# Kernel tuning notes

Hardware: AMD Instinct MI355X
Metric: run time of the kernel (lower is better)

Reference implementation:

```python
import jax, jax.numpy as jnp
import numpy as np

B, S, D = 4, 2048, 1024
H = 16
DK = D // H  # 64, dim_k == dim_v
FF = 4096
EPS = 1e-5


def layer_norm(x, g, b):
    mu = jnp.mean(x, axis=-1, keepdims=True)
    var = jnp.mean(jnp.square(x - mu), axis=-1, keepdims=True)
    return (x - mu) * jax.lax.rsqrt(var + EPS) * g + b


def setup_inputs() -> dict:
    key = jax.random.key(0)
    ks = jax.random.split(key, 16)
    s = 0.02
    return {
        "src": jax.random.normal(ks[0], (B, S, D), jnp.float32),
        # per-head Q/K/V projections (stacked over heads)
        "wq": jax.random.normal(ks[1], (H, D, DK), jnp.float32) * s,
        "bq": jnp.zeros((H, DK), jnp.float32),
        "wk": jax.random.normal(ks[2], (H, D, DK), jnp.float32) * s,
        "bk": jnp.zeros((H, DK), jnp.float32),
        "wv": jax.random.normal(ks[3], (H, D, DK), jnp.float32) * s,
        "bv": jnp.zeros((H, DK), jnp.float32),
        # output projection: concat(H*DK) -> D
        "wo": jax.random.normal(ks[4], (H * DK, D), jnp.float32) * s,
        "bo": jnp.zeros((D,), jnp.float32),
        "ln1_g": jnp.ones((D,), jnp.float32),
        "ln1_b": jnp.zeros((D,), jnp.float32),
        # FFN
        "w1": jax.random.normal(ks[5], (D, FF), jnp.float32) * s,
        "b1": jnp.zeros((FF,), jnp.float32),
        "w2": jax.random.normal(ks[6], (FF, D), jnp.float32) * s,
        "b2": jnp.zeros((D,), jnp.float32),
        "ln2_g": jnp.ones((D,), jnp.float32),
        "ln2_b": jnp.zeros((D,), jnp.float32),
    }


def reference(src, wq, bq, wk, bk, wv, bv, wo, bo, ln1_g, ln1_b,
              w1, b1, w2, b2, ln2_g, ln2_b):
    # per-head projections: [B,S,D] x [H,D,K] -> [B,H,S,K]
    q = jnp.einsum('bsd,hdk->bhsk', src, wq) + bq[None, :, None, :]
    k = jnp.einsum('bsd,hdk->bhsk', src, wk) + bk[None, :, None, :]
    v = jnp.einsum('bsd,hdk->bhsk', src, wv) + bv[None, :, None, :]
    scale = 1.0 / jnp.sqrt(jnp.float32(DK))
    scores = jnp.einsum('bhsk,bhtk->bhst', q, k) * scale  # [B,H,S,S]
    attn = jax.nn.softmax(scores, axis=-1)
    o = jnp.einsum('bhst,bhtv->bhsv', attn, v)            # [B,H,S,DK]
    o = o.transpose(0, 2, 1, 3).reshape(B, S, H * DK)      # concat heads
    attn_out = o @ wo + bo
    x = layer_norm(src + attn_out, ln1_g, ln1_b)
    ff = jax.nn.relu(x @ w1 + b1) @ w2 + b2
    return layer_norm(x + ff, ln2_g, ln2_b)
```

## Files before the change

kernel.cpp:

```cpp
#include <hip/hip_runtime.h>

typedef __bf16 bf16;
typedef __bf16 bf16x8 __attribute__((ext_vector_type(8)));
typedef __bf16 bf16x4 __attribute__((ext_vector_type(4)));
typedef float  f32x4  __attribute__((ext_vector_type(4)));
typedef float  f32x16 __attribute__((ext_vector_type(16)));
typedef unsigned int u32;
typedef int i32x2 __attribute__((ext_vector_type(2)));

#define NB 4
#define NS 2048
#define ND 1024
#define NH 16
#define NDK 64
#define NFF 4096
#define NM (NB*NS)

__device__ __forceinline__ void load_lds16(const void* g, void* l) {
  __builtin_amdgcn_global_load_lds(
      (const __attribute__((address_space(1))) void*)g,
      (__attribute__((address_space(3))) void*)l, 16, 0, 0);
}

__device__ __forceinline__ u32 pack2(float a, float b) {
  union { bf16 h[2]; u32 u; } z;
  z.h[0] = (bf16)a; z.h[1] = (bf16)b;
  return z.u;
}

__device__ __forceinline__ i32x2 pswap(u32 a, u32 b) {
#if __has_builtin(__builtin_amdgcn_permlane32_swap)
  return __builtin_amdgcn_permlane32_swap((int)a, (int)b, false, false);
#else
  u32 x = a, y = b;
  asm volatile("v_permlane32_swap_b32 %0, %1" : "+v"(x), "+v"(y));
  i32x2 r; r[0] = (int)x; r[1] = (int)y; return r;
#endif
}

__global__ __launch_bounds__(256)
void cvt_f32_bf16(const float* __restrict__ in, bf16* __restrict__ out, int n) {
  int i = (blockIdx.x * 256 + threadIdx.x) * 4;
  if (i < n) {
    float4 v = *(const float4*)&in[i];
    bf16x4 o;
    o[0] = (bf16)v.x; o[1] = (bf16)v.y; o[2] = (bf16)v.z; o[3] = (bf16)v.w;
    *(bf16x4*)&out[i] = o;
  }
}

__global__ __launch_bounds__(256)
void transpose_cvt(const float* __restrict__ in, bf16* __restrict__ out,
                   int R, int C, size_t in_bs, size_t out_bs) {
  __shared__ float t[32][33];
  int bx = blockIdx.x, by = blockIdx.y, bz = blockIdx.z;
  const float* ip = in + (size_t)bz * in_bs + (size_t)(bx * 32) * C + by * 32;
  bf16* op = out + (size_t)bz * out_bs + (size_t)(by * 32) * R + bx * 32;
  int x = threadIdx.x & 31, y = threadIdx.x >> 5;
#pragma unroll
  for (int yy = 0; yy < 32; yy += 8)
    t[y + yy][x] = ip[(size_t)(y + yy) * C + x];
  __syncthreads();
#pragma unroll
  for (int yy = 0; yy < 32; yy += 8)
    op[(size_t)(y + yy) * R + x] = (bf16)t[x][y + yy];
}

__global__ __launch_bounds__(256)
void transpose_v(const bf16* __restrict__ v, bf16* __restrict__ vT) {
  __shared__ bf16 t[64][72];
  int st = blockIdx.x;
  int bh = blockIdx.y;
  const bf16* ip = v + ((size_t)bh * NS + st * 64) * NDK;
  bf16* op = vT + (size_t)bh * NDK * NS + st * 64;
  int tid = threadIdx.x;
#pragma unroll
  for (int c = tid; c < 512; c += 256) {
    int r = c >> 3, q = c & 7;
    bf16x8 d = *(const bf16x8*)&ip[(size_t)r * NDK + q * 8];
#pragma unroll
    for (int j = 0; j < 8; j++) t[r][q * 8 + j] = d[j];
  }
  __syncthreads();
#pragma unroll
  for (int c = tid; c < 512; c += 256) {
    int dv = c >> 3, sq = c & 7;
    bf16x8 d;
#pragma unroll
    for (int j = 0; j < 8; j++) d[j] = t[sq * 8 + j][dv];
    *(bf16x8*)&op[(size_t)dv * NS + sq * 8] = d;
  }
}

template<int EPI>
__global__ __launch_bounds__(256)
void gemm_bt(const bf16* __restrict__ A, const bf16* __restrict__ Bt,
             const float* __restrict__ bias0, const float* __restrict__ bias1,
             const float* __restrict__ bias2, void* __restrict__ out0,
             int M, int N, int K) {
  __shared__ __align__(16) bf16 lA[128 * 32];
  __shared__ __align__(16) bf16 lB[128 * 32];
  const int tid = threadIdx.x;
  const int lane = tid & 63;
  const int w = tid >> 6;
  const int wr = w >> 1, wc = w & 1;
  const int blane = lane & 15, glane = lane >> 4;
  const int bm = blockIdx.x * 128;
  const int bn = blockIdx.y * 128;

  f32x4 acc[4][4] = {};
  const bf16* aBase = A + (size_t)bm * K;
  const bf16* bBase = Bt + (size_t)bn * K;
  const int c0 = tid, c1 = tid + 256;

  for (int kt = 0; kt < K; kt += 32) {
    const bf16* ag = aBase + kt;
    const bf16* bg = bBase + kt;
    load_lds16(ag + (size_t)(c0 >> 2) * K + (c0 & 3) * 8, &lA[c0 * 8]);
    load_lds16(ag + (size_t)(c1 >> 2) * K + (c1 & 3) * 8, &lA[c1 * 8]);
    load_lds16(bg + (size_t)(c0 >> 2) * K + (c0 & 3) * 8, &lB[c0 * 8]);
    load_lds16(bg + (size_t)(c1 >> 2) * K + (c1 & 3) * 8, &lB[c1 * 8]);
    __syncthreads();
    bf16x8 af[4], bfr[4];
#pragma unroll
    for (int m = 0; m < 4; m++) {
      int row = wr * 64 + m * 16 + blane;
      af[m] = *(const bf16x8*)&lA[row * 32 + glane * 8];
    }
#pragma unroll
    for (int n = 0; n < 4; n++) {
      int row = wc * 64 + n * 16 + blane;
      bfr[n] = *(const bf16x8*)&lB[row * 32 + glane * 8];
    }
#pragma unroll
    for (int m = 0; m < 4; m++)
#pragma unroll
      for (int n = 0; n < 4; n++)
        acc[m][n] = __builtin_amdgcn_mfma_f32_16x16x32_bf16(af[m], bfr[n], acc[m][n], 0, 0, 0);
    __syncthreads();
  }

#pragma unroll
  for (int m = 0; m < 4; m++) {
#pragma unroll
    for (int n = 0; n < 4; n++) {
      int col = bn + wc * 64 + n * 16 + blane;
      if (EPI == 0) {
        int sel = col >> 10;
        int hh = (col & 1023) >> 6;
        int dv = col & 63;
        const float* bp = (sel == 0) ? bias0 : (sel == 1) ? bias1 : bias2;
        float bias = bp[col & 1023];
        bf16* outb = (bf16*)out0 + (size_t)sel * NB * NH * NS * NDK;
#pragma unroll
        for (int i = 0; i < 4; i++) {
          int row = bm + wr * 64 + m * 16 + glane * 4 + i;
          int b_ = row >> 11, s_ = row & 2047;
          outb[(((size_t)(b_ * NH + hh) * NS + s_) * NDK) + dv] = (bf16)(acc[m][n][i] + bias);
        }
      } else if (EPI == 1) {
        float bias = bias0[col];
#pragma unroll
        for (int i = 0; i < 4; i++) {
          int row = bm + wr * 64 + m * 16 + glane * 4 + i;
          float v = acc[m][n][i] + bias;
          v = v > 0.f ? v : 0.f;
          ((bf16*)out0)[(size_t)row * N + col] = (bf16)v;
        }
      } else {
        float bias = bias0[col];
#pragma unroll
        for (int i = 0; i < 4; i++) {
          int row = bm + wr * 64 + m * 16 + glane * 4 + i;
          ((float*)out0)[(size_t)row * N + col] = acc[m][n][i] + bias;
        }
      }
    }
  }
}

__global__ __launch_bounds__(256)
void flash_attn3(const bf16* __restrict__ q, const bf16* __restrict__ k,
                 const bf16* __restrict__ vT, bf16* __restrict__ o) {
  __shared__ __align__(16) bf16 lK[2][64 * 64];
  __shared__ __align__(16) bf16 lV[2][64 * 64];
  const int tid = threadIdx.x, lane = tid & 63, w = tid >> 6;
  const int ql = lane & 31, hi = lane >> 5;
  const int bh = blockIdx.y, qt = blockIdx.x;
  const size_t hb = (size_t)bh * NS * NDK;
  const int qrow = qt * 128 + w * 32 + ql;

  bf16x8 qf[4];
#pragma unroll
  for (int ks = 0; ks < 4; ks++)
    qf[ks] = *(const bf16x8*)&q[hb + (size_t)qrow * NDK + ks * 16 + hi * 8];

  const int r0 = tid >> 3, s0 = ((tid & 7) ^ (r0 & 7)) * 8;
  const int r1 = r0 + 32, s1 = ((tid & 7) ^ (r1 & 7)) * 8;
  const bf16* k0 = k + hb + (size_t)r0 * NDK + s0;
  const bf16* k1 = k + hb + (size_t)r1 * NDK + s1;
  const bf16* v0 = vT + hb + (size_t)r0 * NS + s0;
  const bf16* v1 = vT + hb + (size_t)r1 * NS + s1;

  f32x16 o0 = {}, o1 = {};
  float mR = -3e38f, lR = 0.f;
  const float cl2 = 0.18033688f;

  load_lds16(k0, &lK[0][tid * 8]);
  load_lds16(k1, &lK[0][(tid + 256) * 8]);
  load_lds16(v0, &lV[0][tid * 8]);
  load_lds16(v1, &lV[0][(tid + 256) * 8]);
  __syncthreads();

  const char* lKc = (const char*)&lK[0][0];
  const char* lVc = (const char*)&lV[0][0];
  const int swz = (ql & 7) << 4;

  for (int t = 0; t < NS / 64; t++) {
    const int cur = t & 1;
    if (t < NS / 64 - 1) {
      const size_t ko = (size_t)(t + 1) * 64 * NDK;
      const int vo = (t + 1) * 64;
      load_lds16(k0 + ko, &lK[cur ^ 1][tid * 8]);
      load_lds16(k1 + ko, &lK[cur ^ 1][(tid + 256) * 8]);
      load_lds16(v0 + vo, &lV[cur ^ 1][tid * 8]);
      load_lds16(v1 + vo, &lV[cur ^ 1][(tid + 256) * 8]);
    }
    const char* Kb = lKc + cur * 8192;
    const char* Vb = lVc + cur * 8192;

    f32x16 st0 = {}, st1 = {};
    __builtin_amdgcn_s_setprio(1);
#pragma unroll
    for (int ks = 0; ks < 4; ks++) {
      int byt = (32 * ks + 16 * hi) ^ swz;
      bf16x8 kf0 = *(const bf16x8*)(Kb + ql * 128 + byt);
      bf16x8 kf1 = *(const bf16x8*)(Kb + (32 + ql) * 128 + byt);
      st0 = __builtin_amdgcn_mfma_f32_32x32x16_bf16(kf0, qf[ks], st0, 0, 0, 0);
      st1 = __builtin_amdgcn_mfma_f32_32x32x16_bf16(kf1, qf[ks], st1, 0, 0, 0);
    }
    __builtin_amdgcn_s_setprio(0);

    float mx = st0[0];
#pragma unroll
    for (int r = 1; r < 16; r++) mx = fmaxf(mx, st0[r]);
#pragma unroll
    for (int r = 0; r < 16; r++) mx = fmaxf(mx, st1[r]);
    {
      i32x2 xr = pswap((u32)__float_as_int(mx), (u32)__float_as_int(mx));
      float prt = __int_as_float(hi ? xr[0] : xr[1]);
      mx = fmaxf(mx, prt);
    }

    if (!__all((mx - mR) * cl2 <= 8.0f)) {
      float mn = fmaxf(mR, mx);
      float al = exp2f((mR - mn) * cl2);
      lR *= al;
#pragma unroll
      for (int r = 0; r < 16; r++) { o0[r] *= al; o1[r] *= al; }
      mR = mn;
    }
    float cmn = mR * cl2;
    float ls = 0.f;
#pragma unroll
    for (int r = 0; r < 16; r++) { float p = exp2f(fmaf(st0[r], cl2, -cmn)); st0[r] = p; ls += p; }
#pragma unroll
    for (int r = 0; r < 16; r++) { float p = exp2f(fmaf(st1[r], cl2, -cmn)); st1[r] = p; ls += p; }
    {
      i32x2 sr = pswap((u32)__float_as_int(ls), (u32)__float_as_int(ls));
      float lsp = __int_as_float(hi ? sr[0] : sr[1]);
      float lo_ = hi ? lsp : ls, hi_ = hi ? ls : lsp;
      lR += lo_ + hi_;
    }

#pragma unroll
    for (int tt = 0; tt < 2; tt++) {
      f32x16 stv = (tt == 0) ? st0 : st1;
      u32 wv[8];
#pragma unroll
      for (int i = 0; i < 8; i++) wv[i] = pack2(stv[2 * i], stv[2 * i + 1]);
#pragma unroll
      for (int kk = 0; kk < 2; kk++) {
        const int base = 4 * kk;
        i32x2 e0 = pswap(wv[base + 0], wv[base + 2]);
        i32x2 e1 = pswap(wv[base + 1], wv[base + 3]);
        union { u32 u[4]; bf16x8 v; } pf;
        pf.u[0] = (u32)e0[0];
        pf.u[1] = (u32)e1[0];
        pf.u[2] = (u32)e0[1];
        pf.u[3] = (u32)e1[1];
        const int ks = 2 * tt + kk;
        int vbyt = (32 * ks + 16 * hi) ^ swz;
        bf16x8 vf0 = *(const bf16x8*)(Vb + ql * 128 + vbyt);
        bf16x8 vf1 = *(const bf16x8*)(Vb + (32 + ql) * 128 + vbyt);
        __builtin_amdgcn_s_setprio(1);
        o0 = __builtin_amdgcn_mfma_f32_32x32x16_bf16(vf0, pf.v, o0, 0, 0, 0);
        o1 = __builtin_amdgcn_mfma_f32_32x32x16_bf16(vf1, pf.v, o1, 0, 0, 0);
        __builtin_amdgcn_s_setprio(0);
      }
    }
    __syncthreads();
  }

  float invl = 1.0f / lR;
  int b_ = bh >> 4, h_ = bh & 15;
  bf16* ob = o + ((size_t)(b_ * NS + qrow) * (NH * NDK)) + h_ * NDK;
#pragma unroll
  for (int rp = 0; rp < 8; rp++) {
    int dv = 8 * (rp >> 1) + 2 * (rp & 1) + 4 * hi;
    *(u32*)&ob[dv]      = pack2(o0[2 * rp] * invl, o0[2 * rp + 1] * invl);
    *(u32*)&ob[dv + 32] = pack2(o1[2 * rp] * invl, o1[2 * rp + 1] * invl);
  }
}

template<int WB>
__global__ __launch_bounds__(256)
void ln_res(const float* __restrict__ a, const float* __restrict__ b,
            const float* __restrict__ g, const float* __restrict__ be,
            float* __restrict__ y, bf16* __restrict__ yb) {
  int row = blockIdx.x;
  int tid = threadIdx.x;
  const float4* a4 = (const float4*)(a + (size_t)row * ND);
  const float4* b4 = (const float4*)(b + (size_t)row * ND);
  float4 av = a4[tid], bv = b4[tid];
  float x0 = av.x + bv.x, x1 = av.y + bv.y, x2 = av.z + bv.z, x3 = av.w + bv.w;
  float s = x0 + x1 + x2 + x3;
  float qq_ = x0 * x0 + x1 * x1 + x2 * x2 + x3 * x3;
#pragma unroll
  for (int d = 1; d < 64; d <<= 1) { s += __shfl_xor(s, d); qq_ += __shfl_xor(qq_, d); }
  __shared__ float ss[4], sq[4];
  int w = tid >> 6, lane = tid & 63;
  if (lane == 0) { ss[w] = s; sq[w] = qq_; }
  __syncthreads();
  s = ss[0] + ss[1] + ss[2] + ss[3];
  qq_ = sq[0] + sq[1] + sq[2] + sq[3];
  float mu = s * (1.0f / ND);
  float var = qq_ * (1.0f / ND) - mu * mu;
  float rs = 1.0f / sqrtf(var + 1e-5f);
  const float4* g4 = (const float4*)g;
  const float4* e4 = (const float4*)be;
  float4 gv = g4[tid], ev = e4[tid];
  float o0 = (x0 - mu) * rs * gv.x + ev.x;
  float o1 = (x1 - mu) * rs * gv.y + ev.y;
  float o2 = (x2 - mu) * rs * gv.z + ev.z;
  float o3 = (x3 - mu) * rs * gv.w + ev.w;
  float4 ov = {o0, o1, o2, o3};
  *(float4*)(y + (size_t)row * ND + tid * 4) = ov;
  if (WB) {
    bf16x4 wv;
    wv[0] = (bf16)o0; wv[1] = (bf16)o1; wv[2] = (bf16)o2; wv[3] = (bf16)o3;
    *(bf16x4*)&yb[(size_t)row * ND + tid * 4] = wv;
  }
}

extern "C" void kernel_launch(void* const* d_in, const int* in_sizes, int n_in,
                              void* d_out, int out_size, void* d_ws, size_t ws_size,
                              hipStream_t stream) {
  const float* src = (const float*)d_in[0];
  const float* wq  = (const float*)d_in[1];
  const float* bq  = (const float*)d_in[2];
  const float* wk  = (const float*)d_in[3];
  const float* bk  = (const float*)d_in[4];
  const float* wv  = (const float*)d_in[5];
  const float* bv  = (const float*)d_in[6];
  const float* wo  = (const float*)d_in[7];
  const float* bo  = (const float*)d_in[8];
  const float* g1  = (const float*)d_in[9];
  const float* be1 = (const float*)d_in[10];
  const float* w1  = (const float*)d_in[11];
  const float* b1  = (const float*)d_in[12];
  const float* w2  = (const float*)d_in[13];
  const float* b2  = (const float*)d_in[14];
  const float* g2  = (const float*)d_in[15];
  const float* be2 = (const float*)d_in[16];

  char* ws = (char*)d_ws;
  bf16*  srcb  = (bf16*)(ws + 0);
  bf16*  wqkvT = (bf16*)(ws + 16777216);
  bf16*  woT   = (bf16*)(ws + 23068672);
  bf16*  w1T   = (bf16*)(ws + 25165824);
  bf16*  w2T   = (bf16*)(ws + 33554432);
  bf16*  qkv   = (bf16*)(ws + 41943040);
  bf16*  vT    = (bf16*)(ws + 92274688);
  bf16*  attno = (bf16*)(ws + 109051904);
  float* tmpf  = (float*)(ws + 125829120);
  float* x     = (float*)(ws + 159383552);
  bf16*  xb    = (bf16*)(ws + 192937984);
  bf16*  hbuf  = qkv;

  const size_t QKVSZ = (size_t)NB * NH * NS * NDK;

  cvt_f32_bf16<<<8192, 256, 0, stream>>>(src, srcb, NM * ND);
  transpose_cvt<<<dim3(32, 2, 16), 256, 0, stream>>>(wq, wqkvT,               1024, 64, 65536, 65536);
  transpose_cvt<<<dim3(32, 2, 16), 256, 0, stream>>>(wk, wqkvT + 1024 * 1024, 1024, 64, 65536, 65536);
  transpose_cvt<<<dim3(32, 2, 16), 256, 0, stream>>>(wv, wqkvT + 2048 * 1024, 1024, 64, 65536, 65536);
  transpose_cvt<<<dim3(32, 32, 1), 256, 0, stream>>>(wo, woT, 1024, 1024, 0, 0);
  transpose_cvt<<<dim3(32, 128, 1), 256, 0, stream>>>(w1, w1T, 1024, 4096, 0, 0);
  transpose_cvt<<<dim3(128, 32, 1), 256, 0, stream>>>(w2, w2T, 4096, 1024, 0, 0);

  gemm_bt<0><<<dim3(64, 24), 256, 0, stream>>>(srcb, wqkvT, bq, bk, bv, qkv, NM, 3072, 1024);
  transpose_v<<<dim3(32, 64), 256, 0, stream>>>(qkv + 2 * QKVSZ, vT);
  flash_attn3<<<dim3(16, 64), 256, 0, stream>>>(qkv, qkv + QKVSZ, vT, attno);
  gemm_bt<2><<<dim3(64, 8), 256, 0, stream>>>(attno, woT, bo, nullptr, nullptr, tmpf, NM, 1024, 1024);
  ln_res<1><<<8192, 256, 0, stream>>>(src, tmpf, g1, be1, x, xb);
  gemm_bt<1><<<dim3(64, 32), 256, 0, stream>>>(xb, w1T, b1, nullptr, nullptr, hbuf, NM, 4096, 1024);
  gemm_bt<2><<<dim3(64, 8), 256, 0, stream>>>(hbuf, w2T, b2, nullptr, nullptr, tmpf, NM, 1024, 4096);
  ln_res<0><<<8192, 256, 0, stream>>>(x, tmpf, g2, be2, (float*)d_out, nullptr);
}
```

Measured before the change: 523.5 us.

## Replace GEMM kernel with 256-row tiled, double-buffered, 8-wave pipelined MFMA GEMM

Replaces the simple 128x128 single-buffered GEMM with a 512-thread kernel using 256xBN tiles, K=64 steps, double-buffered LDS with XOR swizzling, and an interleaved schedule of LDS loads, global-to-LDS prefetch and MFMA quarters separated by barriers and setprio hints. It also remaps blocks in an XCD-aware order to improve L2 locality. This targets memory latency and LDS bank conflicts in all four projection and FFN GEMMs. The cost is much higher register and LDS pressure, plus a hand-tuned vmcnt schedule that relies on exact load counts.

```diff
diff --git a/kernel.cpp b/kernel.cpp
--- a/kernel.cpp
+++ b/kernel.cpp
@@ -92,59 +92,137 @@
   }
 }
 
-template<int EPI>
-__global__ __launch_bounds__(256)
-void gemm_bt(const bf16* __restrict__ A, const bf16* __restrict__ Bt,
-             const float* __restrict__ bias0, const float* __restrict__ bias1,
-             const float* __restrict__ bias2, void* __restrict__ out0,
-             int M, int N, int K) {
-  __shared__ __align__(16) bf16 lA[128 * 32];
-  __shared__ __align__(16) bf16 lB[128 * 32];
-  const int tid = threadIdx.x;
-  const int lane = tid & 63;
-  const int w = tid >> 6;
-  const int wr = w >> 1, wc = w & 1;
+#define BAR()  __builtin_amdgcn_s_barrier()
+#define LGKM0() do { asm volatile("s_waitcnt lgkmcnt(0)" ::: "memory"); \
+                     __builtin_amdgcn_sched_barrier(0); } while (0)
+
+template<int BN, int EPI>
+__global__ __launch_bounds__(512, 2)
+void gemm8p(const bf16* __restrict__ A, const bf16* __restrict__ Bt,
+            const float* __restrict__ bias0, const float* __restrict__ bias1,
+            const float* __restrict__ bias2, void* __restrict__ out0,
+            int M, int N, int K) {
+  constexpr int NFR = BN / 64;
+  __shared__ __align__(16) bf16 lA[2][256 * 64];
+  __shared__ __align__(16) bf16 lB[2][BN * 64];
+
+  const int tid = threadIdx.x, lane = tid & 63, w = tid >> 6;
+  const int wr = w >> 2, wn = w & 3;
   const int blane = lane & 15, glane = lane >> 4;
-  const int bm = blockIdx.x * 128;
-  const int bn = blockIdx.y * 128;
-
-  f32x4 acc[4][4] = {};
-  const bf16* aBase = A + (size_t)bm * K;
-  const bf16* bBase = Bt + (size_t)bn * K;
-  const int c0 = tid, c1 = tid + 256;
-
-  for (int kt = 0; kt < K; kt += 32) {
-    const bf16* ag = aBase + kt;
-    const bf16* bg = bBase + kt;
-    load_lds16(ag + (size_t)(c0 >> 2) * K + (c0 & 3) * 8, &lA[c0 * 8]);
-    load_lds16(ag + (size_t)(c1 >> 2) * K + (c1 & 3) * 8, &lA[c1 * 8]);
-    load_lds16(bg + (size_t)(c0 >> 2) * K + (c0 & 3) * 8, &lB[c0 * 8]);
-    load_lds16(bg + (size_t)(c1 >> 2) * K + (c1 & 3) * 8, &lB[c1 * 8]);
-    __syncthreads();
-    bf16x8 af[4], bfr[4];
-#pragma unroll
-    for (int m = 0; m < 4; m++) {
-      int row = wr * 64 + m * 16 + blane;
-      af[m] = *(const bf16x8*)&lA[row * 32 + glane * 8];
-    }
-#pragma unroll
-    for (int n = 0; n < 4; n++) {
-      int row = wc * 64 + n * 16 + blane;
-      bfr[n] = *(const bf16x8*)&lB[row * 32 + glane * 8];
-    }
-#pragma unroll
-    for (int m = 0; m < 4; m++)
-#pragma unroll
-      for (int n = 0; n < 4; n++)
-        acc[m][n] = __builtin_amdgcn_mfma_f32_16x16x32_bf16(af[m], bfr[n], acc[m][n], 0, 0, 0);
-    __syncthreads();
-  }
-
-#pragma unroll
-  for (int m = 0; m < 4; m++) {
-#pragma unroll
-    for (int n = 0; n < 4; n++) {
-      int col = bn + wc * 64 + n * 16 + blane;
+
+  const int nwg = gridDim.x;
+  const int cpx = nwg >> 3;
+  const int bid = blockIdx.x;
+  const int swzb = (bid & 7) * cpx + (bid >> 3);
+  const int gridM = M >> 8;
+  const int bm = (swzb % gridM) * 256;
+  const int bn = (swzb / gridM) * BN;
+
+  f32x4 acc[8][NFR] = {};
+  bf16x8 aF[8], bF[2 * NFR];
+
+  auto stageA = [&](int kt, int h, int b) {
+#pragma unroll
+    for (int j = 0; j < 2; j++) {
+      int ch = w * 128 + j * 64 + lane;
+      int r = h * 128 + (ch >> 3), s = ch & 7;
+      load_lds16(A + (size_t)(bm + r) * K + kt * 64 + ((s ^ (r & 7)) * 8),
+                 &lA[b][(h * 1024 + ch) * 8]);
+    }
+  };
+  auto stageB = [&](int kt, int h, int b) {
+    if constexpr (BN == 256) {
+#pragma unroll
+      for (int j = 0; j < 2; j++) {
+        int ch = w * 128 + j * 64 + lane;
+        int r = h * 128 + (ch >> 3), s = ch & 7;
+        load_lds16(Bt + (size_t)(bn + r) * K + kt * 64 + ((s ^ (r & 7)) * 8),
+                   &lB[b][(h * 1024 + ch) * 8]);
+      }
+    } else {
+      int ch = w * 64 + lane;
+      int r = h * 64 + (ch >> 3), s = ch & 7;
+      load_lds16(Bt + (size_t)(bn + r) * K + kt * 64 + ((s ^ (r & 7)) * 8),
+                 &lB[b][(h * 512 + ch) * 8]);
+    }
+  };
+  auto vmwait = [&]() {
+    if constexpr (BN == 256) asm volatile("s_waitcnt vmcnt(6)" ::: "memory");
+    else                     asm volatile("s_waitcnt vmcnt(4)" ::: "memory");
+  };
+  auto ldA = [&](int mh, int b) {
+#pragma unroll
+    for (int mf = 0; mf < 4; mf++)
+#pragma unroll
+      for (int ks = 0; ks < 2; ks++) {
+        int r = wr * 128 + mh * 64 + mf * 16 + blane;
+        int s = (ks * 4 + glane) ^ (r & 7);
+        aF[mf * 2 + ks] = *(const bf16x8*)&lA[b][r * 64 + s * 8];
+      }
+  };
+  auto ldB = [&](int b) {
+#pragma unroll
+    for (int nf = 0; nf < NFR; nf++)
+#pragma unroll
+      for (int ks = 0; ks < 2; ks++) {
+        int r = wn * (NFR * 16) + nf * 16 + blane;
+        int s = (ks * 4 + glane) ^ (r & 7);
+        bF[nf * 2 + ks] = *(const bf16x8*)&lB[b][r * 64 + s * 8];
+      }
+  };
+
+#define MMAQ(mh, nh)  do {                                                  \
+    __builtin_amdgcn_s_setprio(1);                                          \
+    _Pragma("unroll")                                                       \
+    for (int mf = 0; mf < 4; mf++)                                          \
+      _Pragma("unroll")                                                     \
+      for (int nq = 0; nq < NFR / 2; nq++)                                  \
+        _Pragma("unroll")                                                   \
+        for (int ks = 0; ks < 2; ks++)                                      \
+          acc[(mh) * 4 + mf][(nh) * (NFR / 2) + nq] =                       \
+            __builtin_amdgcn_mfma_f32_16x16x32_bf16(                        \
+              aF[mf * 2 + ks], bF[((nh) * (NFR / 2) + nq) * 2 + ks],        \
+              acc[(mh) * 4 + mf][(nh) * (NFR / 2) + nq], 0, 0, 0);          \
+    __builtin_amdgcn_s_setprio(0);                                          \
+  } while (0)
+
+  stageB(0, 0, 0); stageB(0, 1, 0); stageA(0, 0, 0); stageA(0, 1, 0);
+  stageB(1, 0, 1); stageB(1, 1, 1); stageA(1, 0, 1);
+  vmwait();
+  BAR();
+
+  const int NT = K >> 6;
+  for (int u = 0; u < NT; u += 2) {
+    const int t2 = (u + 2 < NT) ? u + 2 : u;
+    const int t3 = (u + 3 < NT) ? u + 3 : u + 1;
+    ldA(0, 0); ldB(0);
+    stageA(u + 1, 1, 1);
+    BAR(); LGKM0(); MMAQ(0, 0); BAR();
+    stageB(t2, 0, 0);
+    BAR(); MMAQ(0, 1); BAR();
+    ldA(1, 0);
+    stageB(t2, 1, 0);
+    BAR(); LGKM0(); MMAQ(1, 1); BAR();
+    stageA(t2, 0, 0);
+    BAR(); MMAQ(1, 0); vmwait(); BAR();
+    ldA(0, 1); ldB(1);
+    stageA(t2, 1, 0);
+    BAR(); LGKM0(); MMAQ(0, 0); BAR();
+    stageB(t3, 0, 1);
+    BAR(); MMAQ(0, 1); BAR();
+    ldA(1, 1);
+    stageB(t3, 1, 1);
+    BAR(); LGKM0(); MMAQ(1, 1); BAR();
+    stageA(t3, 0, 1);
+    BAR(); MMAQ(1, 0); vmwait(); BAR();
+  }
+
+#pragma unroll
+  for (int am = 0; am < 8; am++) {
+#pragma unroll
+    for (int nf = 0; nf < NFR; nf++) {
+      int col = bn + wn * (NFR * 16) + nf * 16 + blane;
+      int rowb = bm + wr * 128 + (am >> 2) * 64 + (am & 3) * 16 + glane * 4;
       if (EPI == 0) {
         int sel = col >> 10;
         int hh = (col & 1023) >> 6;
@@ -154,29 +232,27 @@
         bf16* outb = (bf16*)out0 + (size_t)sel * NB * NH * NS * NDK;
 #pragma unroll
         for (int i = 0; i < 4; i++) {
-          int row = bm + wr * 64 + m * 16 + glane * 4 + i;
+          int row = rowb + i;
           int b_ = row >> 11, s_ = row & 2047;
-          outb[(((size_t)(b_ * NH + hh) * NS + s_) * NDK) + dv] = (bf16)(acc[m][n][i] + bias);
+          outb[(((size_t)(b_ * NH + hh) * NS + s_) * NDK) + dv] = (bf16)(acc[am][nf][i] + bias);
         }
       } else if (EPI == 1) {
         float bias = bias0[col];
 #pragma unroll
         for (int i = 0; i < 4; i++) {
-          int row = bm + wr * 64 + m * 16 + glane * 4 + i;
-          float v = acc[m][n][i] + bias;
+          float v = acc[am][nf][i] + bias;
           v = v > 0.f ? v : 0.f;
-          ((bf16*)out0)[(size_t)row * N + col] = (bf16)v;
+          ((bf16*)out0)[(size_t)(rowb + i) * N + col] = (bf16)v;
         }
       } else {
         float bias = bias0[col];
 #pragma unroll
-        for (int i = 0; i < 4; i++) {
-          int row = bm + wr * 64 + m * 16 + glane * 4 + i;
-          ((float*)out0)[(size_t)row * N + col] = acc[m][n][i] + bias;
-        }
+        for (int i = 0; i < 4; i++)
+          ((float*)out0)[(size_t)(rowb + i) * N + col] = acc[am][nf][i] + bias;
       }
     }
   }
+#undef MMAQ
 }
 
 __global__ __launch_bounds__(256)
@@ -398,12 +474,12 @@
   transpose_cvt<<<dim3(32, 128, 1), 256, 0, stream>>>(w1, w1T, 1024, 4096, 0, 0);
   transpose_cvt<<<dim3(128, 32, 1), 256, 0, stream>>>(w2, w2T, 4096, 1024, 0, 0);
 
-  gemm_bt<0><<<dim3(64, 24), 256, 0, stream>>>(srcb, wqkvT, bq, bk, bv, qkv, NM, 3072, 1024);
+  gemm8p<256, 0><<<384, 512, 0, stream>>>(srcb, wqkvT, bq, bk, bv, qkv, NM, 3072, 1024);
   transpose_v<<<dim3(32, 64), 256, 0, stream>>>(qkv + 2 * QKVSZ, vT);
   flash_attn3<<<dim3(16, 64), 256, 0, stream>>>(qkv, qkv + QKVSZ, vT, attno);
-  gemm_bt<2><<<dim3(64, 8), 256, 0, stream>>>(attno, woT, bo, nullptr, nullptr, tmpf, NM, 1024, 1024);
+  gemm8p<128, 2><<<256, 512, 0, stream>>>(attno, woT, bo, nullptr, nullptr, tmpf, NM, 1024, 1024);
   ln_res<1><<<8192, 256, 0, stream>>>(src, tmpf, g1, be1, x, xb);
-  gemm_bt<1><<<dim3(64, 32), 256, 0, stream>>>(xb, w1T, b1, nullptr, nullptr, hbuf, NM, 4096, 1024);
-  gemm_bt<2><<<dim3(64, 8), 256, 0, stream>>>(hbuf, w2T, b2, nullptr, nullptr, tmpf, NM, 1024, 4096);
+  gemm8p<256, 1><<<512, 512, 0, stream>>>(xb, w1T, b1, nullptr, nullptr, hbuf, NM, 4096, 1024);
+  gemm8p<128, 2><<<256, 512, 0, stream>>>(hbuf, w2T, b2, nullptr, nullptr, tmpf, NM, 1024, 4096);
   ln_res<0><<<8192, 256, 0, stream>>>(x, tmpf, g2, be2, (float*)d_out, nullptr);
 }
```

New measurement: 496.3 us. 1.05x faster.
